# Kernel tuning notes

Hardware: AMD Instinct MI355X
Metric: run time of the kernel (lower is better)

Reference implementation:

```python
import math
import jax, jax.numpy as jnp
import numpy as np

B, L, D, H = 256, 32, 512, 512
NEG_INF = -1e9


def setup_inputs() -> dict:
    key = jax.random.key(0)
    ks = jax.random.split(key, 7)
    x = jax.random.normal(ks[0], (B, L, D), dtype=jnp.float32)
    length = jax.random.randint(ks[1], (B,), 2, L + 1)  # valid lengths in [2, L]
    # word_linear: D -> 2H
    W_word = jax.random.normal(ks[2], (2 * H, D), dtype=jnp.float32) * (1.0 / math.sqrt(D))
    b_word = jnp.zeros((2 * H,), dtype=jnp.float32)
    # comp_linear: 2H -> 5H (orthogonal-ish init; scale is fine for a reference)
    W_comp = jax.random.normal(ks[3], (5 * H, 2 * H), dtype=jnp.float32) * (1.0 / math.sqrt(2 * H))
    b_comp = jnp.zeros((5 * H,), dtype=jnp.float32)
    comp_query = jax.random.normal(ks[4], (H,), dtype=jnp.float32) * 0.01
    return {"x": x, "length": length, "W_word": W_word, "b_word": b_word,
            "W_comp": W_comp, "b_comp": b_comp, "comp_query": comp_query}


def _treelstm_compose(hl, cl, hr, cr, W_comp, b_comp):
    # hl/hr: [B, n, H] -> parent h, c: [B, n, H]
    v = jnp.einsum('bnd,kd->bnk', jnp.concatenate([hl, hr], axis=2), W_comp) + b_comp
    i, fl, fr, u, o = jnp.split(v, 5, axis=2)
    c = cl * jax.nn.sigmoid(fl + 1.0) + cr * jax.nn.sigmoid(fr + 1.0) \
        + jnp.tanh(u) * jax.nn.sigmoid(i)
    h = jax.nn.sigmoid(o) * jnp.tanh(c)
    return h, c


def reference(x, length, W_word, b_word, W_comp, b_comp, comp_query):
    length_mask = (jnp.arange(L)[None, :] < length[:, None]).astype(jnp.float32)  # [B, L]
    # leaf states from word_linear (use_leaf_rnn=False path)
    hc = jnp.einsum('bld,kd->blk', x, W_word) + b_word  # [B, L, 2H]
    h, c = jnp.split(hc, 2, axis=2)
    scale = 1.0 / math.sqrt(H)
    for i in range(L - 1):
        new_h, new_c = _treelstm_compose(h[:, :-1], c[:, :-1], h[:, 1:], c[:, 1:], W_comp, b_comp)
        if i < L - 2:
            # eval-mode greedy composition selection (basic.greedy_select)
            logits = jnp.sum(comp_query * new_h, axis=-1) * scale  # [B, L-1-i]
            mask = length_mask[:, i + 1:]
            logits = jnp.where(mask > 0, logits, NEG_INF)
            select = jax.nn.one_hot(jnp.argmax(logits, axis=1), logits.shape[1], dtype=jnp.float32)
            cum = jnp.cumsum(select, axis=1)
            left = (1.0 - cum)[:, :, None]
            right = (cum - select)[:, :, None]
            sel = select[:, :, None]
            new_h = sel * new_h + left * h[:, :-1] + right * h[:, 1:]
            new_c = sel * new_c + left * c[:, :-1] + right * c[:, 1:]
        done = length_mask[:, i + 1][:, None, None]
        h = done * new_h + (1.0 - done) * h[:, :-1]
        c = done * new_c + (1.0 - done) * c[:, :-1]
    return h[:, 0, :]  # final root hidden state [B, H]
```

## Files before the change

kernel.cpp:

```cpp
#include <hip/hip_runtime.h>
#include <cmath>

#define B_   256
#define L_   32
#define H_   512
#define NH5  2560
#define N2   5120
#define SCALE 0.044194173824159216f

__device__ float g_h [B_*L_*H_];
__device__ float g_c [B_*L_*H_];
__device__ float g_al[(size_t)B_*L_*NH5];
__device__ float g_ar[(size_t)B_*L_*NH5];
__device__ float g_logit[B_*L_];
__device__ int   g_list[B_*L_];
__device__ int   g_count[B_];
__device__ int   g_merged[B_];
__device__ int   g_mpos[B_];
__device__ int   g_off[B_];
__device__ int   g_rows[B_*L_];
__device__ int   g_nrows;
__device__ int   g_mlist[2][B_];
__device__ int   g_cnt[2];

__device__ __forceinline__ float sigm(float x) { return 1.0f / (1.0f + expf(-x)); }

__global__ __launch_bounds__(256) void scan_init(const int* __restrict__ length) {
  __shared__ int sw[4];
  const int t = threadIdx.x;
  const int len = length[t];
  int v = len;
#pragma unroll
  for (int off = 1; off < 64; off <<= 1) {
    int o = __shfl_up(v, off, 64);
    if ((t & 63) >= off) v += o;
  }
  if ((t & 63) == 63) sw[t >> 6] = v;
  __syncthreads();
  int base = 0;
  for (int w = 0; w < (t >> 6); w++) base += sw[w];
  const int incl = base + v;
  g_off[t] = incl - len;
  if (t == 255) g_nrows = incl;
  g_count[t] = len; g_merged[t] = -2; g_mpos[t] = 0;
  if (t == 0) { g_cnt[0] = 0; g_cnt[1] = 0; }
}

__global__ __launch_bounds__(32) void fill_rows() {
  const int b = blockIdx.x, t = threadIdx.x;
  g_list[b*L_ + t] = t;
  if (t < g_count[b]) g_rows[g_off[b] + t] = b*L_ + t;
}

template<int MODE>
__global__ __launch_bounds__(256) void gemm_big(
    const float* __restrict__ Aext,
    const float* __restrict__ Bm,
    const float* __restrict__ bias)
{
  const int NR = g_nrows;
  const int m0 = blockIdx.y * 128;
  if (m0 >= NR) return;
  const int n0 = blockIdx.x * 128;

  const int tid = threadIdx.x;
  const int w = tid >> 6, l = tid & 63;
  const int tx = (w & 1) * 8 + (l & 7);
  const int ty = (w >> 1) * 8 + (l >> 3);

  __shared__ float As[8][128];
  __shared__ float Bs[8][128];

  const int ra = tid >> 1, qa = (tid & 1) * 4;

  const float* Abase = (MODE == 0) ? Aext : g_h;
  int mr = m0 + ra; if (mr >= NR) mr = NR - 1;
  const float* aptr = Abase + (size_t)g_rows[mr] * 512 + qa;

  const float* bptr;
  {
    int nrow = n0 + ra;
    if (MODE == 0) bptr = Bm + (size_t)nrow * 512 + qa;
    else bptr = Bm + (nrow < NH5 ? (size_t)nrow * 1024
                                 : (size_t)(nrow - NH5) * 1024 + 512) + qa;
  }

  float4 av = *(const float4*)(aptr);
  float4 bv = *(const float4*)(bptr);
  float acc[8][8] = {};

  for (int k0 = 0; k0 < 512; k0 += 8) {
    __syncthreads();
    As[qa+0][ra] = av.x; As[qa+1][ra] = av.y; As[qa+2][ra] = av.z; As[qa+3][ra] = av.w;
    Bs[qa+0][ra] = bv.x; Bs[qa+1][ra] = bv.y; Bs[qa+2][ra] = bv.z; Bs[qa+3][ra] = bv.w;
    __syncthreads();
    if (k0 + 8 < 512) {
      av = *(const float4*)(aptr + k0 + 8);
      bv = *(const float4*)(bptr + k0 + 8);
    }
#pragma unroll
    for (int k = 0; k < 8; k++) {
      float af[8], bf[8];
#pragma unroll
      for (int c = 0; c < 2; c++) {
        float4 t = *(const float4*)&As[k][ty*8 + 4*c];
        af[4*c+0]=t.x; af[4*c+1]=t.y; af[4*c+2]=t.z; af[4*c+3]=t.w;
      }
#pragma unroll
      for (int c = 0; c < 2; c++) {
        float4 t = *(const float4*)&Bs[k][tx*8 + 4*c];
        bf[4*c+0]=t.x; bf[4*c+1]=t.y; bf[4*c+2]=t.z; bf[4*c+3]=t.w;
      }
#pragma unroll
      for (int i = 0; i < 8; i++)
#pragma unroll
        for (int j = 0; j < 8; j++)
          acc[i][j] = fmaf(af[i], bf[j], acc[i][j]);
    }
  }

#pragma unroll
  for (int i = 0; i < 8; i++) {
    int mrow = m0 + ty*8 + i;
    if (mrow >= NR) continue;
    int crow = g_rows[mrow];
#pragma unroll
    for (int j = 0; j < 8; j++) {
      int n = n0 + tx*8 + j;
      float v = acc[i][j];
      if (MODE == 0) {
        v += bias[n];
        if (n < H_) g_h[(size_t)crow*H_ + n]        = v;
        else        g_c[(size_t)crow*H_ + (n - H_)] = v;
      } else {
        if (n < NH5) g_al[(size_t)crow*NH5 + n]         = v;
        else         g_ar[(size_t)crow*NH5 + (n - NH5)] = v;
      }
    }
  }
}

__global__ __launch_bounds__(256) void iter0_logits(const int* __restrict__ length,
                                                    const float* __restrict__ bc,
                                                    const float* __restrict__ qv) {
  __shared__ float sred[4];
  const int p = blockIdx.x, b = blockIdx.y;
  if (p >= length[b] - 1) return;
  const float* al = g_al + (size_t)(b*L_ + p)*NH5;
  const float* ar = g_ar + (size_t)(b*L_ + p + 1)*NH5;
  const float* cl = g_c  + (size_t)(b*L_ + p)*H_;
  const float* cr = g_c  + (size_t)(b*L_ + p + 1)*H_;
  float part = 0.f;
#pragma unroll
  for (int jj = 0; jj < H_/256; jj++) {
    int j = threadIdx.x + jj*256;
    float vi  = al[j]       + ar[j]       + bc[j];
    float vfl = al[H_+j]    + ar[H_+j]    + bc[H_+j];
    float vfr = al[2*H_+j]  + ar[2*H_+j]  + bc[2*H_+j];
    float vu  = al[3*H_+j]  + ar[3*H_+j]  + bc[3*H_+j];
    float vo  = al[4*H_+j]  + ar[4*H_+j]  + bc[4*H_+j];
    float c = cl[j]*sigm(vfl+1.f) + cr[j]*sigm(vfr+1.f) + tanhf(vu)*sigm(vi);
    float h = sigm(vo)*tanhf(c);
    part = fmaf(qv[j], h, part);
  }
#pragma unroll
  for (int off = 32; off; off >>= 1) part += __shfl_down(part, off, 64);
  if ((threadIdx.x & 63) == 0) sred[threadIdx.x >> 6] = part;
  __syncthreads();
  if (threadIdx.x == 0)
    g_logit[b*L_ + p] = (sred[0]+sred[1]+sred[2]+sred[3]) * SCALE;
}

__global__ __launch_bounds__(256) void select_merge(int iter,
    const int* __restrict__ length,
    const float* __restrict__ bc,
    const float* __restrict__ qv)
{
  __shared__ float sred[4];
  __shared__ int s_sel[3];
  const int b = blockIdx.x, tid = threadIdx.x;
  if (b == 0 && tid == 0) g_cnt[(iter & 1) ^ 1] = 0;

  const int m     = g_count[b];
  const int pslot = g_merged[b];
  const int ppos  = g_mpos[b];
  int* list = g_list + b*L_;

  if (iter > 0 && pslot >= 0) {
    const int half = tid >> 7, lt = tid & 127;
    int sl = -1, sr = -1;
    if (half == 0) { if (ppos > 0)     { sl = list[ppos-1]; sr = list[ppos];   } }
    else           { if (ppos < m - 1) { sl = list[ppos];   sr = list[ppos+1]; } }
    float part = 0.f;
    if (sl >= 0) {
      const float* al = g_al + (size_t)(b*L_+sl)*NH5;
      const float* ar = g_ar + (size_t)(b*L_+sr)*NH5;
      const float* cl = g_c  + (size_t)(b*L_+sl)*H_;
      const float* cr = g_c  + (size_t)(b*L_+sr)*H_;
#pragma unroll
      for (int jj = 0; jj < H_/128; jj++) {
        int j = lt + jj*128;
        float vi  = al[j]       + ar[j]       + bc[j];
        float vfl = al[H_+j]    + ar[H_+j]    + bc[H_+j];
        float vfr = al[2*H_+j]  + ar[2*H_+j]  + bc[2*H_+j];
        float vu  = al[3*H_+j]  + ar[3*H_+j]  + bc[3*H_+j];
        float vo  = al[4*H_+j]  + ar[4*H_+j]  + bc[4*H_+j];
        float c = cl[j]*sigm(vfl+1.f) + cr[j]*sigm(vfr+1.f) + tanhf(vu)*sigm(vi);
        float h = sigm(vo)*tanhf(c);
        part = fmaf(qv[j], h, part);
      }
    }
#pragma unroll
    for (int off = 32; off; off >>= 1) part += __shfl_down(part, off, 64);
    if ((tid & 63) == 0) sred[tid >> 6] = part;
    __syncthreads();
    if (tid == 0   && ppos > 0)     g_logit[b*L_ + list[ppos-1]] = (sred[0]+sred[1])*SCALE;
    if (tid == 128 && ppos < m - 1) g_logit[b*L_ + list[ppos]]   = (sred[2]+sred[3])*SCALE;
  }

  const bool active = iter < (length[b] - 1);
  if (!active) { if (tid == 0) g_merged[b] = -1; return; }

  __syncthreads();

  if (tid < 64) {
    float lg = -1e30f; int idx = tid;
    if (tid < m - 1) lg = g_logit[b*L_ + list[tid]];
#pragma unroll
    for (int off = 32; off; off >>= 1) {
      float olg = __shfl_down(lg, off, 64);
      int   oid = __shfl_down(idx, off, 64);
      if (olg > lg || (olg == lg && oid < idx)) { lg = olg; idx = oid; }
    }
    if (tid == 0) { s_sel[0] = idx; s_sel[1] = list[idx]; s_sel[2] = list[idx+1]; }
  }
  __syncthreads();
  const int pos = s_sel[0], sl = s_sel[1], sr = s_sel[2];

  {
    const float* al = g_al + (size_t)(b*L_+sl)*NH5;
    const float* ar = g_ar + (size_t)(b*L_+sr)*NH5;
    float*       cl = g_c  + (size_t)(b*L_+sl)*H_;
    const float* cr = g_c  + (size_t)(b*L_+sr)*H_;
    float*       hl = g_h  + (size_t)(b*L_+sl)*H_;
#pragma unroll
    for (int jj = 0; jj < H_/256; jj++) {
      int j = tid + jj*256;
      float vi  = al[j]       + ar[j]       + bc[j];
      float vfl = al[H_+j]    + ar[H_+j]    + bc[H_+j];
      float vfr = al[2*H_+j]  + ar[2*H_+j]  + bc[2*H_+j];
      float vu  = al[3*H_+j]  + ar[3*H_+j]  + bc[3*H_+j];
      float vo  = al[4*H_+j]  + ar[4*H_+j]  + bc[4*H_+j];
      float c = cl[j]*sigm(vfl+1.f) + cr[j]*sigm(vfr+1.f) + tanhf(vu)*sigm(vi);
      float h = sigm(vo)*tanhf(c);
      cl[j] = c; hl[j] = h;
    }
  }
  if (tid == 0) {
    for (int n = pos+1; n < m-1; n++) list[n] = list[n+1];
    g_count[b]  = m - 1;
    g_merged[b] = sl;
    g_mpos[b]   = pos;
    int k = atomicAdd(&g_cnt[iter & 1], 1);
    g_mlist[iter & 1][k] = b;
  }
}

__global__ __launch_bounds__(256) void gemm_iter(int par, const float* __restrict__ Wc)
{
  const int nact = g_cnt[par];
  const int m0 = blockIdx.y * 32;
  if (m0 >= nact) return;
  const int n0 = blockIdx.x * 64;
  const int tid = threadIdx.x;

  __shared__ float As[32][32];
  __shared__ float Bs[32][64];

  const int ra = tid >> 3, qa = (tid & 7) * 4;
  int mr = m0 + ra; if (mr >= nact) mr = nact - 1;
  const int bbA = g_mlist[par][mr];
  const float* aptr = g_h + (size_t)(bbA*L_ + g_merged[bbA]) * 512 + qa;

  const int rb = tid >> 2, qb = (tid & 3) * 8;
  const int nr = n0 + rb;
  const float* bptr = (nr < NH5) ? Wc + (size_t)nr * 1024 + qb
                                 : Wc + (size_t)(nr - NH5) * 1024 + 512 + qb;

  const int tx = tid & 15, ty = tid >> 4;

  float4 av  = *(const float4*)(aptr);
  float4 bv0 = *(const float4*)(bptr);
  float4 bv1 = *(const float4*)(bptr + 4);
  float acc[2][4] = {};

  for (int k0 = 0; k0 < 512; k0 += 32) {
    __syncthreads();
    As[qa+0][ra] = av.x;  As[qa+1][ra] = av.y;  As[qa+2][ra] = av.z;  As[qa+3][ra] = av.w;
    Bs[qb+0][rb] = bv0.x; Bs[qb+1][rb] = bv0.y; Bs[qb+2][rb] = bv0.z; Bs[qb+3][rb] = bv0.w;
    Bs[qb+4][rb] = bv1.x; Bs[qb+5][rb] = bv1.y; Bs[qb+6][rb] = bv1.z; Bs[qb+7][rb] = bv1.w;
    __syncthreads();
    if (k0 + 32 < 512) {
      av  = *(const float4*)(aptr + k0 + 32);
      bv0 = *(const float4*)(bptr + k0 + 32);
      bv1 = *(const float4*)(bptr + k0 + 36);
    }
#pragma unroll
    for (int k = 0; k < 32; k++) {
      float2 a2 = *(const float2*)&As[k][ty*2];
      float4 b4 = *(const float4*)&Bs[k][tx*4];
      acc[0][0] = fmaf(a2.x, b4.x, acc[0][0]);
      acc[0][1] = fmaf(a2.x, b4.y, acc[0][1]);
      acc[0][2] = fmaf(a2.x, b4.z, acc[0][2]);
      acc[0][3] = fmaf(a2.x, b4.w, acc[0][3]);
      acc[1][0] = fmaf(a2.y, b4.x, acc[1][0]);
      acc[1][1] = fmaf(a2.y, b4.y, acc[1][1]);
      acc[1][2] = fmaf(a2.y, b4.z, acc[1][2]);
      acc[1][3] = fmaf(a2.y, b4.w, acc[1][3]);
    }
  }

#pragma unroll
  for (int i = 0; i < 2; i++) {
    int mrow = m0 + ty*2 + i;
    if (mrow >= nact) continue;
    int bb = g_mlist[par][mrow];
    size_t base = (size_t)(bb*L_ + g_merged[bb]) * NH5;
    int n = n0 + tx*4;
    float4 v = make_float4(acc[i][0], acc[i][1], acc[i][2], acc[i][3]);
    if (n < NH5) *(float4*)(g_al + base + n)         = v;
    else         *(float4*)(g_ar + base + (n - NH5)) = v;
  }
}

__global__ __launch_bounds__(256) void write_out(float* __restrict__ out) {
  int b = blockIdx.x;
  for (int j = threadIdx.x; j < H_; j += 256)
    out[(size_t)b*H_ + j] = g_h[(size_t)(b*L_)*H_ + j];
}

extern "C" void kernel_launch(void* const* d_in, const int* in_sizes, int n_in,
                              void* d_out, int out_size, void* d_ws, size_t ws_size,
                              hipStream_t stream)
{
  (void)in_sizes; (void)n_in; (void)out_size; (void)d_ws; (void)ws_size;
  const float* x      = (const float*)d_in[0];
  const int*   length = (const int*)  d_in[1];
  const float* W_word = (const float*)d_in[2];
  const float* b_word = (const float*)d_in[3];
  const float* W_comp = (const float*)d_in[4];
  const float* b_comp = (const float*)d_in[5];
  const float* q      = (const float*)d_in[6];
  float* out = (float*)d_out;

  scan_init<<<1, 256, 0, stream>>>(length);
  fill_rows<<<B_, 32, 0, stream>>>();

  gemm_big<0><<<dim3(1024/128, 64), 256, 0, stream>>>(x, W_word, b_word);
  gemm_big<1><<<dim3(N2/128,   64), 256, 0, stream>>>(nullptr, W_comp, nullptr);

  iter0_logits<<<dim3(L_-1, B_), 256, 0, stream>>>(length, b_comp, q);

  for (int i = 0; i < L_-1; i++) {
    select_merge<<<B_, 256, 0, stream>>>(i, length, b_comp, q);
    if (i < L_-2)
      gemm_iter<<<dim3(N2/64, 8), 256, 0, stream>>>(i & 1, W_comp);
  }

  write_out<<<B_, 256, 0, stream>>>(out);
}
```

Before: 1.681 ms.

## Fuse per-iteration select/merge and GEMM into one kernel with per-batch flags

Merges the select_merge and gemm_iter kernels into a single launch per iteration. The first 256 blocks do selection and merge, then publish a per-batch flag. GEMM tiles, now indexed directly by batch instead of a compacted active list, spin-wait on the flags for their 32 rows. This removes one launch per iteration and the atomic compaction, and it vectorises the elementwise loads with float4. In exchange, GEMM tiles for batches that are already done still run, and the design relies on the merge blocks being scheduled before or alongside the waiting blocks (launch_bounds 256,3 plus sleep), which carries a risk of deadlock or spinning overhead.

```diff
diff --git a/kernel.cpp b/kernel.cpp
--- a/kernel.cpp
+++ b/kernel.cpp
@@ -20,8 +20,7 @@
 __device__ int   g_off[B_];
 __device__ int   g_rows[B_*L_];
 __device__ int   g_nrows;
-__device__ int   g_mlist[2][B_];
-__device__ int   g_cnt[2];
+__device__ int   g_flag[B_];
 
 __device__ __forceinline__ float sigm(float x) { return 1.0f / (1.0f + expf(-x)); }
 
@@ -42,8 +41,7 @@
   const int incl = base + v;
   g_off[t] = incl - len;
   if (t == 255) g_nrows = incl;
-  g_count[t] = len; g_merged[t] = -2; g_mpos[t] = 0;
-  if (t == 0) { g_cnt[0] = 0; g_cnt[1] = 0; }
+  g_count[t] = len; g_merged[t] = -2; g_mpos[t] = 0; g_flag[t] = 0;
 }
 
 __global__ __launch_bounds__(32) void fill_rows() {
@@ -171,127 +169,166 @@
     g_logit[b*L_ + p] = (sred[0]+sred[1]+sred[2]+sred[3]) * SCALE;
 }
 
-__global__ __launch_bounds__(256) void select_merge(int iter,
+template<bool GEMM>
+__global__ __launch_bounds__(256, 3) void iter_fused(int iter,
     const int* __restrict__ length,
     const float* __restrict__ bc,
-    const float* __restrict__ qv)
+    const float* __restrict__ qv,
+    const float* __restrict__ Wc)
 {
+  const int bid = blockIdx.x, tid = threadIdx.x;
   __shared__ float sred[4];
   __shared__ int s_sel[3];
-  const int b = blockIdx.x, tid = threadIdx.x;
-  if (b == 0 && tid == 0) g_cnt[(iter & 1) ^ 1] = 0;
-
-  const int m     = g_count[b];
-  const int pslot = g_merged[b];
-  const int ppos  = g_mpos[b];
-  int* list = g_list + b*L_;
-
-  if (iter > 0 && pslot >= 0) {
-    const int half = tid >> 7, lt = tid & 127;
-    int sl = -1, sr = -1;
-    if (half == 0) { if (ppos > 0)     { sl = list[ppos-1]; sr = list[ppos];   } }
-    else           { if (ppos < m - 1) { sl = list[ppos];   sr = list[ppos+1]; } }
-    float part = 0.f;
-    if (sl >= 0) {
-      const float* al = g_al + (size_t)(b*L_+sl)*NH5;
-      const float* ar = g_ar + (size_t)(b*L_+sr)*NH5;
-      const float* cl = g_c  + (size_t)(b*L_+sl)*H_;
-      const float* cr = g_c  + (size_t)(b*L_+sr)*H_;
-#pragma unroll
-      for (int jj = 0; jj < H_/128; jj++) {
-        int j = lt + jj*128;
-        float vi  = al[j]       + ar[j]       + bc[j];
-        float vfl = al[H_+j]    + ar[H_+j]    + bc[H_+j];
-        float vfr = al[2*H_+j]  + ar[2*H_+j]  + bc[2*H_+j];
-        float vu  = al[3*H_+j]  + ar[3*H_+j]  + bc[3*H_+j];
-        float vo  = al[4*H_+j]  + ar[4*H_+j]  + bc[4*H_+j];
-        float c = cl[j]*sigm(vfl+1.f) + cr[j]*sigm(vfr+1.f) + tanhf(vu)*sigm(vi);
-        float h = sigm(vo)*tanhf(c);
-        part = fmaf(qv[j], h, part);
-      }
-    }
-#pragma unroll
-    for (int off = 32; off; off >>= 1) part += __shfl_down(part, off, 64);
-    if ((tid & 63) == 0) sred[tid >> 6] = part;
+
+  if (bid < B_) {
+    const int b = bid;
+    const int m     = g_count[b];
+    const int pslot = g_merged[b];
+    const int ppos  = g_mpos[b];
+    int* list = g_list + b*L_;
+
+    if (iter > 0 && pslot >= 0) {
+      const int half = tid >> 7, lt = tid & 127;
+      int sl = -1, sr = -1;
+      if (half == 0) { if (ppos > 0)     { sl = list[ppos-1]; sr = list[ppos];   } }
+      else           { if (ppos < m - 1) { sl = list[ppos];   sr = list[ppos+1]; } }
+      float part = 0.f;
+      if (sl >= 0) {
+        const float* al = g_al + (size_t)(b*L_+sl)*NH5;
+        const float* ar = g_ar + (size_t)(b*L_+sr)*NH5;
+        const float* cl = g_c  + (size_t)(b*L_+sl)*H_;
+        const float* cr = g_c  + (size_t)(b*L_+sr)*H_;
+        const int j = lt * 4;
+        float4 ai  = *(const float4*)(al + j)        , bi  = *(const float4*)(ar + j);
+        float4 afl = *(const float4*)(al + H_   + j) , bfl = *(const float4*)(ar + H_   + j);
+        float4 afr = *(const float4*)(al + 2*H_ + j) , bfr = *(const float4*)(ar + 2*H_ + j);
+        float4 au  = *(const float4*)(al + 3*H_ + j) , bu  = *(const float4*)(ar + 3*H_ + j);
+        float4 ao  = *(const float4*)(al + 4*H_ + j) , bo  = *(const float4*)(ar + 4*H_ + j);
+        float4 c4l = *(const float4*)(cl + j)        , c4r = *(const float4*)(cr + j);
+        float4 q4  = *(const float4*)(qv + j);
+        const float* bc0 = bc + j;
+        {
+          float c, h;
+          c = c4l.x*sigm(afl.x+bfl.x+bc0[H_]+1.f)   + c4r.x*sigm(afr.x+bfr.x+bc0[2*H_]+1.f)
+            + tanhf(au.x+bu.x+bc0[3*H_])*sigm(ai.x+bi.x+bc0[0]);
+          h = sigm(ao.x+bo.x+bc0[4*H_])*tanhf(c);   part = fmaf(q4.x, h, part);
+          c = c4l.y*sigm(afl.y+bfl.y+bc0[H_+1]+1.f) + c4r.y*sigm(afr.y+bfr.y+bc0[2*H_+1]+1.f)
+            + tanhf(au.y+bu.y+bc0[3*H_+1])*sigm(ai.y+bi.y+bc0[1]);
+          h = sigm(ao.y+bo.y+bc0[4*H_+1])*tanhf(c); part = fmaf(q4.y, h, part);
+          c = c4l.z*sigm(afl.z+bfl.z+bc0[H_+2]+1.f) + c4r.z*sigm(afr.z+bfr.z+bc0[2*H_+2]+1.f)
+            + tanhf(au.z+bu.z+bc0[3*H_+2])*sigm(ai.z+bi.z+bc0[2]);
+          h = sigm(ao.z+bo.z+bc0[4*H_+2])*tanhf(c); part = fmaf(q4.z, h, part);
+          c = c4l.w*sigm(afl.w+bfl.w+bc0[H_+3]+1.f) + c4r.w*sigm(afr.w+bfr.w+bc0[2*H_+3]+1.f)
+            + tanhf(au.w+bu.w+bc0[3*H_+3])*sigm(ai.w+bi.w+bc0[3]);
+          h = sigm(ao.w+bo.w+bc0[4*H_+3])*tanhf(c); part = fmaf(q4.w, h, part);
+        }
+      }
+#pragma unroll
+      for (int off = 32; off; off >>= 1) part += __shfl_down(part, off, 64);
+      if ((tid & 63) == 0) sred[tid >> 6] = part;
+      __syncthreads();
+      if (tid == 0   && ppos > 0)     g_logit[b*L_ + list[ppos-1]] = (sred[0]+sred[1])*SCALE;
+      if (tid == 128 && ppos < m - 1) g_logit[b*L_ + list[ppos]]   = (sred[2]+sred[3])*SCALE;
+    }
+
+    const bool active = iter < (length[b] - 1);
+    if (active) {
+      __syncthreads();
+
+      if (tid < 64) {
+        float lg = -1e30f; int idx = tid;
+        if (tid < m - 1) lg = g_logit[b*L_ + list[tid]];
+#pragma unroll
+        for (int off = 32; off; off >>= 1) {
+          float olg = __shfl_down(lg, off, 64);
+          int   oid = __shfl_down(idx, off, 64);
+          if (olg > lg || (olg == lg && oid < idx)) { lg = olg; idx = oid; }
+        }
+        if (tid == 0) { s_sel[0] = idx; s_sel[1] = list[idx]; s_sel[2] = list[idx+1]; }
+      }
+      __syncthreads();
+      const int pos = s_sel[0], sl = s_sel[1], sr = s_sel[2];
+
+      if (tid < 128) {
+        const float* al = g_al + (size_t)(b*L_+sl)*NH5;
+        const float* ar = g_ar + (size_t)(b*L_+sr)*NH5;
+        float*       cl = g_c  + (size_t)(b*L_+sl)*H_;
+        const float* cr = g_c  + (size_t)(b*L_+sr)*H_;
+        float*       hl = g_h  + (size_t)(b*L_+sl)*H_;
+        const int j = tid * 4;
+        float4 ai  = *(const float4*)(al + j)        , bi  = *(const float4*)(ar + j);
+        float4 afl = *(const float4*)(al + H_   + j) , bfl = *(const float4*)(ar + H_   + j);
+        float4 afr = *(const float4*)(al + 2*H_ + j) , bfr = *(const float4*)(ar + 2*H_ + j);
+        float4 au  = *(const float4*)(al + 3*H_ + j) , bu  = *(const float4*)(ar + 3*H_ + j);
+        float4 ao  = *(const float4*)(al + 4*H_ + j) , bo  = *(const float4*)(ar + 4*H_ + j);
+        float4 c4l = *(const float4*)(cl + j)        , c4r = *(const float4*)(cr + j);
+        const float* bc0 = bc + j;
+        float4 cn, hn;
+        cn.x = c4l.x*sigm(afl.x+bfl.x+bc0[H_]+1.f)   + c4r.x*sigm(afr.x+bfr.x+bc0[2*H_]+1.f)
+             + tanhf(au.x+bu.x+bc0[3*H_])*sigm(ai.x+bi.x+bc0[0]);
+        hn.x = sigm(ao.x+bo.x+bc0[4*H_])*tanhf(cn.x);
+        cn.y = c4l.y*sigm(afl.y+bfl.y+bc0[H_+1]+1.f) + c4r.y*sigm(afr.y+bfr.y+bc0[2*H_+1]+1.f)
+             + tanhf(au.y+bu.y+bc0[3*H_+1])*sigm(ai.y+bi.y+bc0[1]);
+        hn.y = sigm(ao.y+bo.y+bc0[4*H_+1])*tanhf(cn.y);
+        cn.z = c4l.z*sigm(afl.z+bfl.z+bc0[H_+2]+1.f) + c4r.z*sigm(afr.z+bfr.z+bc0[2*H_+2]+1.f)
+             + tanhf(au.z+bu.z+bc0[3*H_+2])*sigm(ai.z+bi.z+bc0[2]);
+        hn.z = sigm(ao.z+bo.z+bc0[4*H_+2])*tanhf(cn.z);
+        cn.w = c4l.w*sigm(afl.w+bfl.w+bc0[H_+3]+1.f) + c4r.w*sigm(afr.w+bfr.w+bc0[2*H_+3]+1.f)
+             + tanhf(au.w+bu.w+bc0[3*H_+3])*sigm(ai.w+bi.w+bc0[3]);
+        hn.w = sigm(ao.w+bo.w+bc0[4*H_+3])*tanhf(cn.w);
+        *(float4*)(cl + j) = cn;
+        *(float4*)(hl + j) = hn;
+      }
+      __syncthreads();
+      if (tid == 0) {
+        for (int n = pos+1; n < m-1; n++) list[n] = list[n+1];
+        g_count[b]  = m - 1;
+        g_merged[b] = sl;
+        g_mpos[b]   = pos;
+      }
+    } else {
+      if (tid == 0) g_merged[b] = -1;
+    }
     __syncthreads();
-    if (tid == 0   && ppos > 0)     g_logit[b*L_ + list[ppos-1]] = (sred[0]+sred[1])*SCALE;
-    if (tid == 128 && ppos < m - 1) g_logit[b*L_ + list[ppos]]   = (sred[2]+sred[3])*SCALE;
-  }
-
-  const bool active = iter < (length[b] - 1);
-  if (!active) { if (tid == 0) g_merged[b] = -1; return; }
-
-  __syncthreads();
-
-  if (tid < 64) {
-    float lg = -1e30f; int idx = tid;
-    if (tid < m - 1) lg = g_logit[b*L_ + list[tid]];
-#pragma unroll
-    for (int off = 32; off; off >>= 1) {
-      float olg = __shfl_down(lg, off, 64);
-      int   oid = __shfl_down(idx, off, 64);
-      if (olg > lg || (olg == lg && oid < idx)) { lg = olg; idx = oid; }
-    }
-    if (tid == 0) { s_sel[0] = idx; s_sel[1] = list[idx]; s_sel[2] = list[idx+1]; }
-  }
-  __syncthreads();
-  const int pos = s_sel[0], sl = s_sel[1], sr = s_sel[2];
-
-  {
-    const float* al = g_al + (size_t)(b*L_+sl)*NH5;
-    const float* ar = g_ar + (size_t)(b*L_+sr)*NH5;
-    float*       cl = g_c  + (size_t)(b*L_+sl)*H_;
-    const float* cr = g_c  + (size_t)(b*L_+sr)*H_;
-    float*       hl = g_h  + (size_t)(b*L_+sl)*H_;
-#pragma unroll
-    for (int jj = 0; jj < H_/256; jj++) {
-      int j = tid + jj*256;
-      float vi  = al[j]       + ar[j]       + bc[j];
-      float vfl = al[H_+j]    + ar[H_+j]    + bc[H_+j];
-      float vfr = al[2*H_+j]  + ar[2*H_+j]  + bc[2*H_+j];
-      float vu  = al[3*H_+j]  + ar[3*H_+j]  + bc[3*H_+j];
-      float vo  = al[4*H_+j]  + ar[4*H_+j]  + bc[4*H_+j];
-      float c = cl[j]*sigm(vfl+1.f) + cr[j]*sigm(vfr+1.f) + tanhf(vu)*sigm(vi);
-      float h = sigm(vo)*tanhf(c);
-      cl[j] = c; hl[j] = h;
-    }
-  }
-  if (tid == 0) {
-    for (int n = pos+1; n < m-1; n++) list[n] = list[n+1];
-    g_count[b]  = m - 1;
-    g_merged[b] = sl;
-    g_mpos[b]   = pos;
-    int k = atomicAdd(&g_cnt[iter & 1], 1);
-    g_mlist[iter & 1][k] = b;
-  }
-}
-
-__global__ __launch_bounds__(256) void gemm_iter(int par, const float* __restrict__ Wc)
-{
-  const int nact = g_cnt[par];
-  const int m0 = blockIdx.y * 32;
-  if (m0 >= nact) return;
-  const int n0 = blockIdx.x * 64;
-  const int tid = threadIdx.x;
+    if (tid == 0) {
+      __threadfence();
+      atomicExch(&g_flag[b], iter + 1);
+    }
+  }
+
+  if (!GEMM) return;
+
+  const int mtile = bid / 80;
+  const int ntile = bid % 80;
+  const int m0 = mtile * 32, n0 = ntile * 64;
 
   __shared__ float As[32][32];
   __shared__ float Bs[32][64];
-
-  const int ra = tid >> 3, qa = (tid & 7) * 4;
-  int mr = m0 + ra; if (mr >= nact) mr = nact - 1;
-  const int bbA = g_mlist[par][mr];
-  const float* aptr = g_h + (size_t)(bbA*L_ + g_merged[bbA]) * 512 + qa;
+  __shared__ int s_slot[32];
 
   const int rb = tid >> 2, qb = (tid & 3) * 8;
   const int nr = n0 + rb;
   const float* bptr = (nr < NH5) ? Wc + (size_t)nr * 1024 + qb
                                  : Wc + (size_t)(nr - NH5) * 1024 + 512 + qb;
-
-  const int tx = tid & 15, ty = tid >> 4;
-
-  float4 av  = *(const float4*)(aptr);
   float4 bv0 = *(const float4*)(bptr);
   float4 bv1 = *(const float4*)(bptr + 4);
+
+  if (tid < 32) {
+    while (atomicAdd(&g_flag[m0 + tid], 0) < iter + 1)
+      __builtin_amdgcn_s_sleep(2);
+  }
+  __syncthreads();
+  __threadfence();
+  if (tid < 32) s_slot[tid] = g_merged[m0 + tid];
+  __syncthreads();
+
+  const int ra = tid >> 3, qa = (tid & 7) * 4;
+  const int slotA = (s_slot[ra] >= 0) ? s_slot[ra] : 0;
+  const float* aptr = g_h + (size_t)((m0 + ra)*L_ + slotA) * 512 + qa;
+
+  const int tx = tid & 15, ty = tid >> 4;
+
+  float4 av = *(const float4*)(aptr);
   float acc[2][4] = {};
 
   for (int k0 = 0; k0 < 512; k0 += 32) {
@@ -322,10 +359,10 @@
 
 #pragma unroll
   for (int i = 0; i < 2; i++) {
-    int mrow = m0 + ty*2 + i;
-    if (mrow >= nact) continue;
-    int bb = g_mlist[par][mrow];
-    size_t base = (size_t)(bb*L_ + g_merged[bb]) * NH5;
+    const int mrow = ty*2 + i;
+    const int slot = s_slot[mrow];
+    if (slot < 0) continue;
+    size_t base = (size_t)((m0 + mrow)*L_ + slot) * NH5;
     int n = n0 + tx*4;
     float4 v = make_float4(acc[i][0], acc[i][1], acc[i][2], acc[i][3]);
     if (n < NH5) *(float4*)(g_al + base + n)         = v;
@@ -361,11 +398,9 @@
 
   iter0_logits<<<dim3(L_-1, B_), 256, 0, stream>>>(length, b_comp, q);
 
-  for (int i = 0; i < L_-1; i++) {
-    select_merge<<<B_, 256, 0, stream>>>(i, length, b_comp, q);
-    if (i < L_-2)
-      gemm_iter<<<dim3(N2/64, 8), 256, 0, stream>>>(i & 1, W_comp);
-  }
+  for (int i = 0; i < L_-2; i++)
+    iter_fused<true><<<640, 256, 0, stream>>>(i, length, b_comp, q, W_comp);
+  iter_fused<false><<<B_, 256, 0, stream>>>(L_-2, length, b_comp, q, W_comp);
 
   write_out<<<B_, 256, 0, stream>>>(out);
 }
```

Result: slower. 3.354 ms (+99.6%).
